# Kernel tuning notes

Measured on AMD Instinct MI355X. Metric: run time of the kernel, lower is better.

Reference implementation:

```python
import jax, jax.numpy as jnp
from jax import lax
import numpy as np

K = 5      # window_size; must equal 2*PAD+1 for the unfold/view chain to be shape-consistent
PAD = 2    # hardcoded padding=2 in the original NMS helpers
NUM = 8    # num_attentions == out_channels
RF = 1.0   # reserve_filter
EPS = 1e-5 # BatchNorm eps


def _bn(x, g, b, m, v):
    # inference-mode BatchNorm2d over channel dim of NCHW
    return g[None, :, None, None] * (x - m[None, :, None, None]) * lax.rsqrt(v[None, :, None, None] + EPS) + b[None, :, None, None]


def setup_inputs() -> dict:
    key = jax.random.key(0)
    k = jax.random.split(key, 12)
    B, Cin, Cout, H, W = 8, 64, 8, 128, 128
    x = jax.random.normal(k[0], (B, Cin, H, W), jnp.float32)
    w1 = jax.random.normal(k[1], (Cin, Cin, 3, 3), jnp.float32) * 0.05
    b1 = jax.random.normal(k[2], (Cin,), jnp.float32) * 0.05
    gamma1 = 1.0 + 0.1 * jax.random.normal(k[3], (Cin,), jnp.float32)
    beta1 = 0.1 * jax.random.normal(k[4], (Cin,), jnp.float32)
    mean1 = 0.1 * jax.random.normal(k[5], (Cin,), jnp.float32)
    var1 = jax.random.uniform(k[6], (Cin,), jnp.float32, minval=0.5, maxval=1.5)
    w2 = jax.random.normal(k[7], (Cout, Cin, 1, 1), jnp.float32) * 0.05
    gamma2 = 1.0 + 0.1 * jax.random.normal(k[8], (Cout,), jnp.float32)
    beta2 = 0.1 * jax.random.normal(k[9], (Cout,), jnp.float32)
    mean2 = 0.1 * jax.random.normal(k[10], (Cout,), jnp.float32)
    var2 = jax.random.uniform(k[11], (Cout,), jnp.float32, minval=0.5, maxval=1.5)
    return dict(x=x, w1=w1, b1=b1, gamma1=gamma1, beta1=beta1, mean1=mean1, var1=var1,
                w2=w2, gamma2=gamma2, beta2=beta2, mean2=mean2, var2=var2)


def reference(x, w1, b1, gamma1, beta1, mean1, var1, w2, gamma2, beta2, mean2, var2):
    B, C, H, W = x.shape
    dn = ('NCHW', 'OIHW', 'NCHW')
    x = jax.image.resize(x, (B, C, 2 * H, 2 * W), method='bilinear')
    # conv_extract 3x3 same + BN + ReLU
    x = lax.conv_general_dilated(x, w1, (1, 1), ((1, 1), (1, 1)), dimension_numbers=dn) + b1[None, :, None, None]
    x = jax.nn.relu(_bn(x, gamma1, beta1, mean1, var1))
    # conv2 1x1 (no bias) + BN
    x = lax.conv_general_dilated(x, w2, (1, 1), ((0, 0), (0, 0)), dimension_numbers=dn)
    x = _bn(x, gamma2, beta2, mean2, var2)
    # reserve filter
    xf = jnp.where(x > RF, x, jnp.zeros_like(x))
    # sliding_window_sum: KxK sum with zero pad; output same size since 2*PAD = K-1
    pcfg = ((0, 0), (0, 0), (PAD, PAD), (PAD, PAD))
    ws = lax.reduce_window(xf, 0.0, lax.add, (1, 1, K, K), (1, 1, 1, 1), pcfg)
    # NMS: keep only local maxima of the windowed sum (max_pool2d pads with -inf)
    mp = lax.reduce_window(ws, -jnp.inf, lax.max, (1, 1, K, K), (1, 1, 1, 1), pcfg)
    masked = ws * (ws == mp).astype(ws.dtype)
    Bc, Cc, Hn, Wn = masked.shape
    _, idx = lax.top_k(masked.reshape(Bc, Cc, Hn * Wn), NUM)  # (B, Cout, NUM)
    # extract_top_windows: each flat index l corresponds to the window whose
    # top-left in the zero-padded input is (l // Wn, l % Wn)
    xp = jnp.pad(xf, pcfg)
    h = idx // Wn
    w = idx % Wn
    d = jnp.arange(K)
    Wp = Wn + 2 * PAD
    flat_idx = (h[..., None, None] + d[:, None]) * Wp + (w[..., None, None] + d[None, :])  # (B,C,NUM,K,K)
    patches = jnp.take_along_axis(xp.reshape(Bc, Cc, -1), flat_idx.reshape(Bc, Cc, NUM * K * K), axis=2)
    patches = patches.reshape(Bc, Cc, NUM, K, K)
    # positions (x1, y1, x2, y2), clamped to the feature map
    kk = K // 2
    x1 = jnp.clip(w - kk, 0, Wn - 1)
    y1 = jnp.clip(h - kk, 0, Hn - 1)
    x2 = jnp.clip(w + kk, 0, Wn - 1)
    y2 = jnp.clip(h + kk, 0, Hn - 1)
    positions = jnp.stack([x1, y1, x2, y2], axis=3)  # (B, Cout, NUM, 4)
    return patches, positions
```

## Files before the change

kernel.cpp:

```cpp
#include <hip/hip_runtime.h>
#include <math.h>

#define EPS 1e-5f

typedef __attribute__((ext_vector_type(8))) short short8;
typedef __attribute__((ext_vector_type(4))) float float4v;

__device__ __forceinline__ bool better(float v1, int i1, float v2, int i2) {
  return (v1 > v2) || (v1 == v2 && i1 < i2);
}

__device__ __forceinline__ unsigned short f2bf(float f) {
  unsigned int u = __float_as_uint(f);
  unsigned int r = u + 0x7fffu + ((u >> 16) & 1u);
  return (unsigned short)(r >> 16);
}
__device__ __forceinline__ float bf2f(unsigned short s) {
  return __uint_as_float(((unsigned int)s) << 16);
}

__device__ __constant__ float RCtab[4][3][3] = {
  {{0.75f, 0.25f, 0.f}, {0.25f, 0.75f, 0.f}, {0.f, 0.75f, 0.25f}},
  {{0.25f, 0.75f, 0.f}, {0.f, 0.75f, 0.25f}, {0.f, 0.25f, 0.75f}},
  {{0.f, 0.f, 0.f},     {1.0f, 0.f, 0.f},    {0.75f, 0.25f, 0.f}},
  {{0.f, 0.25f, 0.75f}, {0.f, 0.f, 1.0f},    {0.f, 0.f, 0.f}},
};

__global__ __launch_bounds__(256) void k_wprep(const float* __restrict__ w1,
                                               unsigned short* __restrict__ Wphase,
                                               float* __restrict__ EdgeEff) {
  int e = blockIdx.x * 256 + threadIdx.x;
  if (e < 147456) {
    int cil = e & 31, co = (e >> 5) & 63, ck = (e >> 11) & 1;
    int tap = (e >> 12) % 9, ph = e / 36864;
    int pr = ph >> 1, pc = ph & 1;
    int dr = tap / 3, dc = tap % 3;
    int ci = ck * 32 + cil;
    const float* wp = w1 + (co * 64 + ci) * 9;
    float eff = 0.f;
    #pragma unroll
    for (int kr = 0; kr < 3; ++kr)
      #pragma unroll
      for (int kc = 0; kc < 3; ++kc)
        eff += wp[kr * 3 + kc] * RCtab[pr][kr][dr] * RCtab[pc][kc][dc];
    unsigned short hi = f2bf(eff);
    unsigned short lo = f2bf(eff - bf2f(hi));
    int g = (ph * 9 + tap) * 2 + ck;
    Wphase[g * 4096 + co * 32 + cil] = hi;
    Wphase[g * 4096 + 2048 + co * 32 + cil] = lo;
  } else if (e < 147456 + 589824) {
    int e2 = e - 147456;
    int co = e2 & 63, tap = (e2 >> 6) % 9, ci = (e2 / 576) & 63, set = e2 / 36864;
    int rs = set >> 2, cs = set & 3;
    int dr = tap / 3, dc = tap % 3;
    const float* wp = w1 + (co * 64 + ci) * 9;
    float eff = 0.f;
    #pragma unroll
    for (int kr = 0; kr < 3; ++kr)
      #pragma unroll
      for (int kc = 0; kc < 3; ++kc)
        eff += wp[kr * 3 + kc] * RCtab[rs][kr][dr] * RCtab[cs][kc][dc];
    EdgeEff[set * 36864 + (ci * 9 + tap) * 64 + co] = eff;
  }
}

__global__ __launch_bounds__(256, 1) void k_front(
    const float* __restrict__ x, const unsigned short* __restrict__ Wphase,
    const float* __restrict__ b1, const float* __restrict__ g1,
    const float* __restrict__ be1, const float* __restrict__ m1,
    const float* __restrict__ v1, const float* __restrict__ w2,
    const float* __restrict__ g2, const float* __restrict__ be2,
    const float* __restrict__ m2, const float* __restrict__ v2,
    float* __restrict__ xf)
{
  __shared__ __align__(16) char lds[66560];
  unsigned short* XS = (unsigned short*)lds;
  float* V = (float*)lds;
  __shared__ float w2s[512];
  __shared__ float A1s[64], C1s[64];
  __shared__ float s2s[8], sh2s[8];

  const int tid = threadIdx.x;
  const int bx = blockIdx.x, by = blockIdx.y, bz = blockIdx.z;

  for (int i = tid; i < 512; i += 256) w2s[i] = w2[i];
  if (tid < 64) {
    float sc = g1[tid] * rsqrtf(v1[tid] + EPS);
    A1s[tid] = sc;
    C1s[tid] = sc * (b1[tid] - m1[tid]) + be1[tid];
  }
  if (tid < 8) {
    float sc = g2[tid] * rsqrtf(v2[tid] + EPS);
    s2s[tid] = sc;
    sh2s[tid] = be2[tid] - m2[tid] * sc;
  }

  if (tid < 200) {
    int ckh = tid / 100;
    int pos = tid % 100;
    int r = pos / 10, c = pos % 10;
    int rr = min(max(by * 8 - 1 + r, 0), 127);
    int cc = min(max(bx * 8 - 1 + c, 0), 127);
    #pragma unroll
    for (int b = 0; b < 2; ++b) {
      const float* xp = x + (size_t)((bz * 2 + b) * 64 + ckh * 32) * 16384 + rr * 128 + cc;
      unsigned int* dh = (unsigned int*)(XS + ((b * 2 + ckh) * 2 + 0) * 4000) + pos * 20;
      unsigned int* dl = (unsigned int*)(XS + ((b * 2 + ckh) * 2 + 1) * 4000) + pos * 20;
      for (int cp = 0; cp < 16; ++cp) {
        float v0 = xp[(size_t)(2 * cp) * 16384];
        float v1x = xp[(size_t)(2 * cp + 1) * 16384];
        unsigned short h0 = f2bf(v0), h1 = f2bf(v1x);
        unsigned short l0 = f2bf(v0 - bf2f(h0)), l1 = f2bf(v1x - bf2f(h1));
        dh[cp] = (unsigned int)h0 | ((unsigned int)h1 << 16);
        dl[cp] = (unsigned int)l0 | ((unsigned int)l1 << 16);
      }
    }
  }
  __syncthreads();

  const int l = tid & 63, wv = tid >> 6;
  const int pr = wv >> 1, pc = wv & 1;
  const int lm = l & 15, q = l >> 4;
  const int arow = lm >> 3, acol = lm & 7;

  float4v acc[2][4][4];
  #pragma unroll
  for (int b = 0; b < 2; ++b)
    #pragma unroll
    for (int mt = 0; mt < 4; ++mt)
      #pragma unroll
      for (int nt = 0; nt < 4; ++nt) acc[b][mt][nt] = (float4v){0.f, 0.f, 0.f, 0.f};

  #pragma unroll
  for (int ck = 0; ck < 2; ++ck) {
    #pragma unroll
    for (int tap = 0; tap < 9; ++tap) {
      const int dr = tap / 3, dc = tap % 3;
      const unsigned short* wb = Wphase + ((wv * 9 + tap) * 2 + ck) * 4096;
      short8 bh[4], bl[4];
      #pragma unroll
      for (int nt = 0; nt < 4; ++nt) {
        int off = (nt * 16 + lm) * 32 + q * 8;
        bh[nt] = *(const short8*)(wb + off);
        bl[nt] = *(const short8*)(wb + 2048 + off);
      }
      #pragma unroll
      for (int b = 0; b < 2; ++b) {
        const unsigned short* XH = XS + ((b * 2 + ck) * 2 + 0) * 4000;
        const unsigned short* XL = XS + ((b * 2 + ck) * 2 + 1) * 4000;
        #pragma unroll
        for (int mt = 0; mt < 4; ++mt) {
          int pos = (mt * 2 + arow + dr) * 10 + acol + dc;
          short8 ah = *(const short8*)(XH + pos * 40 + q * 8);
          short8 al = *(const short8*)(XL + pos * 40 + q * 8);
          #pragma unroll
          for (int nt = 0; nt < 4; ++nt) {
            acc[b][mt][nt] = __builtin_amdgcn_mfma_f32_16x16x32_bf16(ah, bh[nt], acc[b][mt][nt], 0, 0, 0);
            acc[b][mt][nt] = __builtin_amdgcn_mfma_f32_16x16x32_bf16(al, bh[nt], acc[b][mt][nt], 0, 0, 0);
            acc[b][mt][nt] = __builtin_amdgcn_mfma_f32_16x16x32_bf16(ah, bl[nt], acc[b][mt][nt], 0, 0, 0);
          }
        }
      }
    }
  }

  #pragma unroll
  for (int b = 0; b < 2; ++b) {
    __syncthreads();
    #pragma unroll
    for (int mt = 0; mt < 4; ++mt) {
      #pragma unroll
      for (int nt = 0; nt < 4; ++nt) {
        int co = nt * 16 + lm;
        float A = A1s[co], Cc = C1s[co];
        #pragma unroll
        for (int r = 0; r < 4; ++r) {
          int p = mt * 16 + q * 4 + r;
          int ur = 2 * (p >> 3) + pr, uc = 2 * (p & 7) + pc;
          V[(ur * 16 + uc) * 65 + co] = fmaxf(fmaf(A, acc[b][mt][nt][r], Cc), 0.f);
        }
      }
    }
    __syncthreads();
    {
      float a2[8];
      #pragma unroll
      for (int c2 = 0; c2 < 8; ++c2) a2[c2] = 0.f;
      const float* vp = &V[tid * 65];
      for (int co = 0; co < 64; ++co) {
        float xv = vp[co];
        #pragma unroll
        for (int c2 = 0; c2 < 8; ++c2) a2[c2] = fmaf(w2s[c2 * 64 + co], xv, a2[c2]);
      }
      int ur = tid >> 4, uc = tid & 15;
      int batch = bz * 2 + b;
      #pragma unroll
      for (int c2 = 0; c2 < 8; ++c2) {
        float y = fmaf(s2s[c2], a2[c2], sh2s[c2]);
        float o = (y > 1.0f) ? y : 0.f;
        xf[((batch * 8 + c2) * 256 + by * 16 + ur) * 256 + bx * 16 + uc] = o;
      }
    }
  }
}

template<int S_IS_DR>
__device__ __forceinline__ void fix_loop(const float* __restrict__ Ecom,
                                         const float* __restrict__ Xs,
                                         int base, float acc[8]) {
  for (int ci = 0; ci < 64; ++ci) {
    const float* xsrow = Xs + ci * 60;
    float run0[12], run1[12], run2[12];
    #pragma unroll
    for (int j = 0; j < 3; ++j) {
      ((float4*)run0)[j] = ((const float4*)(xsrow + base))[j];
      ((float4*)run1)[j] = ((const float4*)(xsrow + 20 + base))[j];
      ((float4*)run2)[j] = ((const float4*)(xsrow + 40 + base))[j];
    }
    float wt[9];
    #pragma unroll
    for (int tap = 0; tap < 9; ++tap) wt[tap] = Ecom[(ci * 9 + tap) * 64];
    #pragma unroll
    for (int tap = 0; tap < 9; ++tap) {
      const int dr = tap / 3, dc = tap % 3;
      const int s = S_IS_DR ? dr : dc;
      const int d = S_IS_DR ? dc : dr;
      const float* run = (s == 0) ? run0 : ((s == 1) ? run1 : run2);
      #pragma unroll
      for (int k = 0; k < 8; ++k)
        acc[k] = fmaf(wt[tap], run[k + d], acc[k]);
    }
  }
}

__device__ __forceinline__ float corner_acc(const float* __restrict__ Ecor,
                                            const float* __restrict__ Xs,
                                            int pcor) {
  float a = 0.f;
  for (int ci = 0; ci < 64; ++ci) {
    const float* xsrow = Xs + ci * 60;
    #pragma unroll
    for (int tap = 0; tap < 9; ++tap) {
      const int dr = tap / 3, dc = tap % 3;
      a = fmaf(Ecor[(ci * 9 + tap) * 64], xsrow[dr * 20 + pcor + dc], a);
    }
  }
  return a;
}

__global__ __launch_bounds__(256, 1) void k_fix(
    const float* __restrict__ x, const float* __restrict__ EdgeEff,
    const float* __restrict__ b1, const float* __restrict__ g1,
    const float* __restrict__ be1, const float* __restrict__ m1,
    const float* __restrict__ v1, const float* __restrict__ w2,
    const float* __restrict__ g2, const float* __restrict__ be2,
    const float* __restrict__ m2, const float* __restrict__ v2,
    float* __restrict__ xf)
{
  __shared__ __align__(16) float Xs[64 * 60];
  __shared__ float w2s[512];
  __shared__ float A1s[64], C1s[64];
  __shared__ float s2s[8], sh2s[8];

  const int tid = threadIdx.x;
  const int seg = blockIdx.x, line = blockIdx.y, bz = blockIdx.z;
  const bool is01 = (line < 2);

  for (int i = tid; i < 512; i += 256) w2s[i] = w2[i];
  if (tid < 64) {
    float sc = g1[tid] * rsqrtf(v1[tid] + EPS);
    A1s[tid] = sc;
    C1s[tid] = sc * (b1[tid] - m1[tid]) + be1[tid];
  }
  if (tid < 8) {
    float sc = g2[tid] * rsqrtf(v2[tid] + EPS);
    s2s[tid] = sc;
    sh2s[tid] = be2[tid] - m2[tid] * sc;
  }

  const int base0 = seg * 16 - 1;
  for (int e = tid; e < 3840; e += 256) {
    int f = e % 20;
    int slot = (e / 20) % 3;
    int ci = e / 60;
    int row, col;
    if (is01) { row = (line == 0 ? 0 : 125) + slot; col = min(max(base0 + f, 0), 127); }
    else      { col = (line == 2 ? 0 : 125) + slot; row = min(max(base0 + f, 0), 127); }
    Xs[e] = x[(size_t)(bz * 64 + ci) * 16384 + row * 128 + col];
  }
  __syncthreads();

  const int w = tid >> 6, co = tid & 63;
  const int par = w & 1;
  const int base = 8 * (w >> 1);

  int setcom;
  if (line == 0)      setcom = 8 | par;
  else if (line == 1) setcom = 12 | par;
  else if (line == 2) setcom = (par << 2) | 2;
  else                setcom = (par << 2) | 3;

  int uu[8];
  #pragma unroll
  for (int k = 0; k < 8; ++k) uu[k] = seg * 32 + 16 * (w >> 1) + 2 * k + par;

  float acc[8] = {0.f, 0.f, 0.f, 0.f, 0.f, 0.f, 0.f, 0.f};
  const float* Ecom = EdgeEff + setcom * 36864 + co;

  if (is01) fix_loop<1>(Ecom, Xs, base, acc);
  else      fix_loop<0>(Ecom, Xs, base, acc);

  if (is01 && seg == 0 && w == 0) {
    const float* Ecor = EdgeEff + ((line == 0) ? 10 : 14) * 36864 + co;
    acc[0] = corner_acc(Ecor, Xs, 1);
  }
  if (is01 && seg == 7 && w == 3) {
    const float* Ecor = EdgeEff + ((line == 0) ? 11 : 15) * 36864 + co;
    acc[7] = corner_acc(Ecor, Xs, 14);
  }

  #pragma unroll
  for (int k = 0; k < 8; ++k) {
    float v = fmaxf(fmaf(A1s[co], acc[k], C1s[co]), 0.f);
    float part[8];
    #pragma unroll
    for (int c2 = 0; c2 < 8; ++c2) part[c2] = w2s[c2 * 64 + co] * v;
    #pragma unroll
    for (int m = 1; m < 64; m <<= 1) {
      #pragma unroll
      for (int c2 = 0; c2 < 8; ++c2) part[c2] += __shfl_xor(part[c2], m, 64);
    }
    bool valid = is01 || (uu[k] >= 1 && uu[k] <= 254);
    if (co < 8 && valid) {
      float y = fmaf(s2s[co], part[co], sh2s[co]);
      float o = (y > 1.0f) ? y : 0.f;
      int R = (line == 0) ? 0 : (line == 1) ? 255 : uu[k];
      int C = (line == 2) ? 0 : (line == 3) ? 255 : uu[k];
      xf[((bz * 8 + co) * 256 + R) * 256 + C] = o;
    }
  }
}

__global__ __launch_bounds__(256) void k_sep(const float* __restrict__ xf,
                                             float* __restrict__ ws,
                                             float* __restrict__ rm) {
  __shared__ float bufx[20 * 256];
  __shared__ float bufr[20 * 256];
  const int plane = blockIdx.x >> 4;
  const int r0 = (blockIdx.x & 15) * 16;
  const int t = threadIdx.x;
  const float* xp = xf + plane * 65536;

  for (int i = t; i < 20 * 256; i += 256) {
    int rr = r0 - 2 + (i >> 8);
    bufx[i] = ((unsigned)rr < 256u) ? xp[(rr << 8) | (i & 255)] : 0.f;
  }
  __syncthreads();

  #pragma unroll 4
  for (int i = 0; i < 20; ++i) {
    const float* row = bufx + i * 256;
    float s = 0.f;
    #pragma unroll
    for (int d = -2; d <= 2; ++d) {
      int cc = t + d;
      if ((unsigned)cc < 256u) s += row[cc];
    }
    bufr[i * 256 + t] = s;
  }
  __syncthreads();

  #pragma unroll 4
  for (int i = 0; i < 16; ++i) {
    int j = i + 2;
    float s = bufr[(j - 2) * 256 + t] + bufr[(j - 1) * 256 + t] + bufr[j * 256 + t] +
              bufr[(j + 1) * 256 + t] + bufr[(j + 2) * 256 + t];
    bufx[j * 256 + t] = s;
    ws[plane * 65536 + (r0 + i) * 256 + t] = s;
  }
  __syncthreads();

  #pragma unroll 4
  for (int i = 0; i < 16; ++i) {
    int j = i + 2;
    float m = -HUGE_VALF;
    #pragma unroll
    for (int d = -2; d <= 2; ++d) {
      int cc = t + d;
      if ((unsigned)cc < 256u) m = fmaxf(m, bufx[j * 256 + cc]);
    }
    rm[plane * 65536 + (r0 + i) * 256 + t] = m;
  }
}

__global__ __launch_bounds__(256) void k_cand(const float* __restrict__ ws,
                                              const float* __restrict__ rm,
                                              float* __restrict__ candv,
                                              int* __restrict__ candi) {
  __shared__ float cv[256 * 8];
  __shared__ int cidx[256 * 8];
  const int t = threadIdx.x;
  const int plane = blockIdx.x >> 3;
  const int r0 = (blockIdx.x & 7) * 32;
  const float* wsp = ws + plane * 65536;
  const float* rmp = rm + plane * 65536;

  float bv[8]; int bi[8];
  #pragma unroll
  for (int k = 0; k < 8; ++k) { bv[k] = -HUGE_VALF; bi[k] = 0x7fffffff; }

  float w0 = (r0 >= 2) ? rmp[(r0 - 2) * 256 + t] : -HUGE_VALF;
  float w1v = (r0 >= 1) ? rmp[(r0 - 1) * 256 + t] : -HUGE_VALF;
  float w2v = rmp[r0 * 256 + t];
  float w3v = rmp[(r0 + 1) * 256 + t];
  for (int r = r0; r < r0 + 32; ++r) {
    float w4v = (r + 2 < 256) ? rmp[(r + 2) * 256 + t] : -HUGE_VALF;
    float mp = fmaxf(fmaxf(fmaxf(w0, w1v), fmaxf(w2v, w3v)), w4v);
    float wsv = wsp[r * 256 + t];
    float mv = (wsv == mp) ? wsv : 0.f;
    int e = (r << 8) | t;
    if (better(mv, e, bv[7], bi[7])) {
      bv[7] = mv; bi[7] = e;
      #pragma unroll
      for (int k = 7; k > 0; --k) {
        if (better(bv[k], bi[k], bv[k - 1], bi[k - 1])) {
          float tv = bv[k]; bv[k] = bv[k - 1]; bv[k - 1] = tv;
          int ti = bi[k]; bi[k] = bi[k - 1]; bi[k - 1] = ti;
        }
      }
    }
    w0 = w1v; w1v = w2v; w2v = w3v; w3v = w4v;
  }

  #pragma unroll
  for (int k = 0; k < 8; ++k) { cv[t * 8 + k] = bv[k]; cidx[t * 8 + k] = bi[k]; }
  __syncthreads();

  for (int s = 128; s >= 1; s >>= 1) {
    if (t < s) {
      float ov[8]; int oi[8];
      int ia = 0, ib = 0;
      #pragma unroll
      for (int k = 0; k < 8; ++k) {
        float va = cv[t * 8 + ia];       int xa = cidx[t * 8 + ia];
        float vb = cv[(t + s) * 8 + ib]; int xb = cidx[(t + s) * 8 + ib];
        if (better(va, xa, vb, xb)) { ov[k] = va; oi[k] = xa; ++ia; }
        else                        { ov[k] = vb; oi[k] = xb; ++ib; }
      }
      #pragma unroll
      for (int k = 0; k < 8; ++k) { cv[t * 8 + k] = ov[k]; cidx[t * 8 + k] = oi[k]; }
    }
    __syncthreads();
  }

  if (t < 8) {
    candv[blockIdx.x * 8 + t] = cv[t];
    candi[blockIdx.x * 8 + t] = cidx[t];
  }
}

__global__ __launch_bounds__(256) void k_final(const float* __restrict__ candv,
                                               const int* __restrict__ candi,
                                               const float* __restrict__ xf,
                                               float* __restrict__ patches,
                                               float* __restrict__ pos) {
  __shared__ float cvs[64];
  __shared__ int cis[64];
  __shared__ int fidx[8];
  const int t = threadIdx.x;
  const int plane = blockIdx.x;

  if (t < 64) { cvs[t] = candv[plane * 64 + t]; cis[t] = candi[plane * 64 + t]; }
  __syncthreads();
  if (t < 64) {
    float v = cvs[t]; int i = cis[t];
    int rank = 0;
    for (int m = 0; m < 64; ++m)
      if (better(cvs[m], cis[m], v, i)) ++rank;
    if (rank < 8) fidx[rank] = i;
  }
  __syncthreads();

  const float* xfp = xf + plane * 65536;
  if (t < 200) {
    int n = t / 25, e = t % 25;
    int kr = e / 5, kc = e % 5;
    int idx = fidx[n];
    int h = idx >> 8, w = idx & 255;
    int rr = h - 2 + kr, cc = w - 2 + kc;
    float v = ((unsigned)rr < 256u && (unsigned)cc < 256u) ? xfp[rr * 256 + cc] : 0.f;
    patches[plane * 200 + t] = v;
  } else if (t < 232) {
    int qq = t - 200;
    int n = qq >> 2, k = qq & 3;
    int idx = fidx[n];
    int h = idx >> 8, w = idx & 255;
    int val;
    if (k == 0)      val = min(max(w - 2, 0), 255);
    else if (k == 1) val = min(max(h - 2, 0), 255);
    else if (k == 2) val = min(max(w + 2, 0), 255);
    else             val = min(max(h + 2, 0), 255);
    pos[plane * 32 + qq] = (float)val;
  }
}

extern "C" void kernel_launch(void* const* d_in, const int* in_sizes, int n_in,
                              void* d_out, int out_size, void* d_ws, size_t ws_size,
                              hipStream_t stream) {
  (void)in_sizes; (void)n_in; (void)out_size; (void)ws_size;
  const float* x   = (const float*)d_in[0];
  const float* w1  = (const float*)d_in[1];
  const float* b1  = (const float*)d_in[2];
  const float* g1  = (const float*)d_in[3];
  const float* be1 = (const float*)d_in[4];
  const float* m1  = (const float*)d_in[5];
  const float* v1  = (const float*)d_in[6];
  const float* w2  = (const float*)d_in[7];
  const float* g2  = (const float*)d_in[8];
  const float* be2 = (const float*)d_in[9];
  const float* m2  = (const float*)d_in[10];
  const float* v2  = (const float*)d_in[11];

  float* out = (float*)d_out;
  const int PLANE = 8 * 8 * 256 * 256;
  float* xf   = (float*)d_ws;
  float* bufA = xf + PLANE;
  float* bufB = bufA + PLANE;
  float* candv = bufB + PLANE;
  int*   candi = (int*)(candv + 4096);
  unsigned short* Wphase = (unsigned short*)bufA;
  float* EdgeEff = bufA + 147456;

  k_wprep<<<2880, 256, 0, stream>>>(w1, Wphase, EdgeEff);
  k_front<<<dim3(16, 16, 4), 256, 0, stream>>>(x, Wphase, b1, g1, be1, m1, v1,
                                               w2, g2, be2, m2, v2, xf);
  k_fix<<<dim3(8, 4, 8), 256, 0, stream>>>(x, EdgeEff, b1, g1, be1, m1, v1,
                                           w2, g2, be2, m2, v2, xf);
  k_sep<<<1024, 256, 0, stream>>>(xf, bufB, bufA);
  k_cand<<<512, 256, 0, stream>>>(bufB, bufA, candv, candi);
  k_final<<<64, 256, 0, stream>>>(candv, candi, xf, out, out + 12800);
}
```

Baseline: 327.4 us.

## Fuse window-sum, row-max and candidate scan; split front MFMA work across 8 waves

The separable window-sum and row-max kernel is merged with the candidate top-k scan. Each block recomputes the sums and row maxima for its 32 rows plus a halo in shared memory, so the ws and rm planes are no longer written to and re-read from global memory. Separately, k_front now launches 512 threads and splits the M tiles between two wave halves, which halves the accumulators per wave and raises the number of waves hiding MFMA latency. The costs are redundant halo computation (40 rows loaded per 32 output), a large 96KB shared-memory footprint that limits occupancy of the scan kernel, and half the threads sitting idle during the 1x1 conv epilogue.

```diff
diff --git a/kernel.cpp b/kernel.cpp
--- a/kernel.cpp
+++ b/kernel.cpp
@@ -64,7 +64,7 @@
   }
 }
 
-__global__ __launch_bounds__(256, 1) void k_front(
+__global__ __launch_bounds__(512, 1) void k_front(
     const float* __restrict__ x, const unsigned short* __restrict__ Wphase,
     const float* __restrict__ b1, const float* __restrict__ g1,
     const float* __restrict__ be1, const float* __restrict__ m1,
@@ -83,7 +83,7 @@
   const int tid = threadIdx.x;
   const int bx = blockIdx.x, by = blockIdx.y, bz = blockIdx.z;
 
-  for (int i = tid; i < 512; i += 256) w2s[i] = w2[i];
+  if (tid < 512) w2s[tid] = w2[tid];
   if (tid < 64) {
     float sc = g1[tid] * rsqrtf(v1[tid] + EPS);
     A1s[tid] = sc;
@@ -118,18 +118,20 @@
   }
   __syncthreads();
 
-  const int l = tid & 63, wv = tid >> 6;
+  const int l = tid & 63, w = tid >> 6;
+  const int wv = w & 3;
+  const int half = w >> 2;
   const int pr = wv >> 1, pc = wv & 1;
   const int lm = l & 15, q = l >> 4;
   const int arow = lm >> 3, acol = lm & 7;
 
-  float4v acc[2][4][4];
+  float4v acc[2][2][4];
   #pragma unroll
   for (int b = 0; b < 2; ++b)
     #pragma unroll
-    for (int mt = 0; mt < 4; ++mt)
-      #pragma unroll
-      for (int nt = 0; nt < 4; ++nt) acc[b][mt][nt] = (float4v){0.f, 0.f, 0.f, 0.f};
+    for (int mtp = 0; mtp < 2; ++mtp)
+      #pragma unroll
+      for (int nt = 0; nt < 4; ++nt) acc[b][mtp][nt] = (float4v){0.f, 0.f, 0.f, 0.f};
 
   #pragma unroll
   for (int ck = 0; ck < 2; ++ck) {
@@ -149,15 +151,16 @@
         const unsigned short* XH = XS + ((b * 2 + ck) * 2 + 0) * 4000;
         const unsigned short* XL = XS + ((b * 2 + ck) * 2 + 1) * 4000;
         #pragma unroll
-        for (int mt = 0; mt < 4; ++mt) {
-          int pos = (mt * 2 + arow + dr) * 10 + acol + dc;
+        for (int mtp = 0; mtp < 2; ++mtp) {
+          int gmt = half * 2 + mtp;
+          int pos = (gmt * 2 + arow + dr) * 10 + acol + dc;
           short8 ah = *(const short8*)(XH + pos * 40 + q * 8);
           short8 al = *(const short8*)(XL + pos * 40 + q * 8);
           #pragma unroll
           for (int nt = 0; nt < 4; ++nt) {
-            acc[b][mt][nt] = __builtin_amdgcn_mfma_f32_16x16x32_bf16(ah, bh[nt], acc[b][mt][nt], 0, 0, 0);
-            acc[b][mt][nt] = __builtin_amdgcn_mfma_f32_16x16x32_bf16(al, bh[nt], acc[b][mt][nt], 0, 0, 0);
-            acc[b][mt][nt] = __builtin_amdgcn_mfma_f32_16x16x32_bf16(ah, bl[nt], acc[b][mt][nt], 0, 0, 0);
+            acc[b][mtp][nt] = __builtin_amdgcn_mfma_f32_16x16x32_bf16(ah, bh[nt], acc[b][mtp][nt], 0, 0, 0);
+            acc[b][mtp][nt] = __builtin_amdgcn_mfma_f32_16x16x32_bf16(al, bh[nt], acc[b][mtp][nt], 0, 0, 0);
+            acc[b][mtp][nt] = __builtin_amdgcn_mfma_f32_16x16x32_bf16(ah, bl[nt], acc[b][mtp][nt], 0, 0, 0);
           }
         }
       }
@@ -168,21 +171,22 @@
   for (int b = 0; b < 2; ++b) {
     __syncthreads();
     #pragma unroll
-    for (int mt = 0; mt < 4; ++mt) {
+    for (int mtp = 0; mtp < 2; ++mtp) {
+      int gmt = half * 2 + mtp;
       #pragma unroll
       for (int nt = 0; nt < 4; ++nt) {
         int co = nt * 16 + lm;
         float A = A1s[co], Cc = C1s[co];
         #pragma unroll
         for (int r = 0; r < 4; ++r) {
-          int p = mt * 16 + q * 4 + r;
+          int p = gmt * 16 + q * 4 + r;
           int ur = 2 * (p >> 3) + pr, uc = 2 * (p & 7) + pc;
-          V[(ur * 16 + uc) * 65 + co] = fmaxf(fmaf(A, acc[b][mt][nt][r], Cc), 0.f);
+          V[(ur * 16 + uc) * 65 + co] = fmaxf(fmaf(A, acc[b][mtp][nt][r], Cc), 0.f);
         }
       }
     }
     __syncthreads();
-    {
+    if (tid < 256) {
       float a2[8];
       #pragma unroll
       for (int c2 = 0; c2 < 8; ++c2) a2[c2] = 0.f;
@@ -341,82 +345,73 @@
   }
 }
 
-__global__ __launch_bounds__(256) void k_sep(const float* __restrict__ xf,
-                                             float* __restrict__ ws,
-                                             float* __restrict__ rm) {
-  __shared__ float bufx[20 * 256];
-  __shared__ float bufr[20 * 256];
-  const int plane = blockIdx.x >> 4;
-  const int r0 = (blockIdx.x & 15) * 16;
-  const int t = threadIdx.x;
-  const float* xp = xf + plane * 65536;
-
-  for (int i = t; i < 20 * 256; i += 256) {
-    int rr = r0 - 2 + (i >> 8);
-    bufx[i] = ((unsigned)rr < 256u) ? xp[(rr << 8) | (i & 255)] : 0.f;
-  }
-  __syncthreads();
-
-  #pragma unroll 4
-  for (int i = 0; i < 20; ++i) {
-    const float* row = bufx + i * 256;
-    float s = 0.f;
-    #pragma unroll
-    for (int d = -2; d <= 2; ++d) {
-      int cc = t + d;
-      if ((unsigned)cc < 256u) s += row[cc];
-    }
-    bufr[i * 256 + t] = s;
-  }
-  __syncthreads();
-
-  #pragma unroll 4
-  for (int i = 0; i < 16; ++i) {
-    int j = i + 2;
-    float s = bufr[(j - 2) * 256 + t] + bufr[(j - 1) * 256 + t] + bufr[j * 256 + t] +
-              bufr[(j + 1) * 256 + t] + bufr[(j + 2) * 256 + t];
-    bufx[j * 256 + t] = s;
-    ws[plane * 65536 + (r0 + i) * 256 + t] = s;
-  }
-  __syncthreads();
-
-  #pragma unroll 4
-  for (int i = 0; i < 16; ++i) {
-    int j = i + 2;
-    float m = -HUGE_VALF;
-    #pragma unroll
-    for (int d = -2; d <= 2; ++d) {
-      int cc = t + d;
-      if ((unsigned)cc < 256u) m = fmaxf(m, bufx[j * 256 + cc]);
-    }
-    rm[plane * 65536 + (r0 + i) * 256 + t] = m;
-  }
-}
-
-__global__ __launch_bounds__(256) void k_cand(const float* __restrict__ ws,
-                                              const float* __restrict__ rm,
+__global__ __launch_bounds__(256) void k_scan(const float* __restrict__ xf,
                                               float* __restrict__ candv,
                                               int* __restrict__ candi) {
+  __shared__ float bufA[40 * 256];
+  __shared__ float bufB[40 * 256];
   __shared__ float cv[256 * 8];
   __shared__ int cidx[256 * 8];
   const int t = threadIdx.x;
   const int plane = blockIdx.x >> 3;
   const int r0 = (blockIdx.x & 7) * 32;
-  const float* wsp = ws + plane * 65536;
-  const float* rmp = rm + plane * 65536;
+  const float* xp = xf + plane * 65536;
+
+  for (int i = t; i < 40 * 256; i += 256) {
+    int rr = r0 - 4 + (i >> 8);
+    bufA[i] = ((unsigned)rr < 256u) ? xp[(rr << 8) | (i & 255)] : 0.f;
+  }
+  __syncthreads();
+
+  #pragma unroll 4
+  for (int i = 0; i < 40; ++i) {
+    const float* row = bufA + i * 256;
+    float s = 0.f;
+    #pragma unroll
+    for (int d = -2; d <= 2; ++d) {
+      int cc = t + d;
+      if ((unsigned)cc < 256u) s += row[cc];
+    }
+    bufB[i * 256 + t] = s;
+  }
+  __syncthreads();
+
+  #pragma unroll 4
+  for (int jj = 0; jj < 36; ++jj) {
+    float s = bufB[jj * 256 + t] + bufB[(jj + 1) * 256 + t] + bufB[(jj + 2) * 256 + t] +
+              bufB[(jj + 3) * 256 + t] + bufB[(jj + 4) * 256 + t];
+    bufA[jj * 256 + t] = s;
+  }
+  __syncthreads();
+
+  #pragma unroll 4
+  for (int jj = 0; jj < 36; ++jj) {
+    int gr = r0 - 2 + jj;
+    float m = -HUGE_VALF;
+    if ((unsigned)gr < 256u) {
+      #pragma unroll
+      for (int d = -2; d <= 2; ++d) {
+        int cc = t + d;
+        if ((unsigned)cc < 256u) m = fmaxf(m, bufA[jj * 256 + cc]);
+      }
+    }
+    bufB[jj * 256 + t] = m;
+  }
+  __syncthreads();
 
   float bv[8]; int bi[8];
   #pragma unroll
   for (int k = 0; k < 8; ++k) { bv[k] = -HUGE_VALF; bi[k] = 0x7fffffff; }
 
-  float w0 = (r0 >= 2) ? rmp[(r0 - 2) * 256 + t] : -HUGE_VALF;
-  float w1v = (r0 >= 1) ? rmp[(r0 - 1) * 256 + t] : -HUGE_VALF;
-  float w2v = rmp[r0 * 256 + t];
-  float w3v = rmp[(r0 + 1) * 256 + t];
+  float w0 = bufB[0 * 256 + t];
+  float w1v = bufB[1 * 256 + t];
+  float w2v = bufB[2 * 256 + t];
+  float w3v = bufB[3 * 256 + t];
   for (int r = r0; r < r0 + 32; ++r) {
-    float w4v = (r + 2 < 256) ? rmp[(r + 2) * 256 + t] : -HUGE_VALF;
+    int jj = r - r0;
+    float w4v = bufB[(jj + 4) * 256 + t];
     float mp = fmaxf(fmaxf(fmaxf(w0, w1v), fmaxf(w2v, w3v)), w4v);
-    float wsv = wsp[r * 256 + t];
+    float wsv = bufA[(jj + 2) * 256 + t];
     float mv = (wsv == mp) ? wsv : 0.f;
     int e = (r << 8) | t;
     if (better(mv, e, bv[7], bi[7])) {
@@ -532,11 +527,10 @@
   float* EdgeEff = bufA + 147456;
 
   k_wprep<<<2880, 256, 0, stream>>>(w1, Wphase, EdgeEff);
-  k_front<<<dim3(16, 16, 4), 256, 0, stream>>>(x, Wphase, b1, g1, be1, m1, v1,
+  k_front<<<dim3(16, 16, 4), 512, 0, stream>>>(x, Wphase, b1, g1, be1, m1, v1,
                                                w2, g2, be2, m2, v2, xf);
   k_fix<<<dim3(8, 4, 8), 256, 0, stream>>>(x, EdgeEff, b1, g1, be1, m1, v1,
                                            w2, g2, be2, m2, v2, xf);
-  k_sep<<<1024, 256, 0, stream>>>(xf, bufB, bufA);
-  k_cand<<<512, 256, 0, stream>>>(bufB, bufA, candv, candi);
+  k_scan<<<512, 256, 0, stream>>>(xf, candv, candi);
   k_final<<<64, 256, 0, stream>>>(candv, candi, xf, out, out + 12800);
 }
```

Measured after the change: 374.7 us. +14.4%, slower.
